# Performance work log

Hardware: AMD Instinct MI355X
Metric: run time of the kernel (lower is better)

## Reference

```python
import jax, jax.numpy as jnp
import numpy as np

BETA = 0.25  # commitment weight from __init__ default
K, D = 512, 64


def setup_inputs() -> dict:
    key = jax.random.key(0)
    k1, k2 = jax.random.split(key)
    latents = jax.random.normal(k1, (32, 64, 64, 64), dtype=jnp.float32)  # [B, D, H, W]
    # nn.Embedding weight initialized uniform(-1/K, 1/K)
    emb_weight = jax.random.uniform(k2, (K, D), dtype=jnp.float32, minval=-1.0 / K, maxval=1.0 / K)
    return {"latents": latents, "emb_weight": emb_weight, "validation": 1}


def reference(latents, emb_weight, validation):
    B, Dc, H, W = latents.shape
    lat = jnp.transpose(latents, (0, 2, 3, 1))          # [B, H, W, D]
    flat = lat.reshape(-1, Dc)                           # [N, D]
    # pairwise squared distances via sum-of-squares + matmul (as in source)
    dist = (jnp.sum(flat * flat, axis=1, keepdims=True)
            + jnp.sum(emb_weight * emb_weight, axis=1)
            - 2.0 * flat @ emb_weight.T)                 # [N, K]
    inds = jnp.argmin(dist, axis=1)                      # [N]
    # one_hot @ emb_weight == gather
    q = emb_weight[inds].reshape(B, H, W, Dc)            # [B, H, W, D]
    commitment_loss = jnp.mean((jax.lax.stop_gradient(q) - lat) ** 2)
    embedding_loss = jnp.mean((q - jax.lax.stop_gradient(lat)) ** 2)
    # eloss starts at 0.0 (and stays 0 in validation), so topology terms vanish
    vq_loss = commitment_loss * BETA + embedding_loss
    # straight-through estimator
    q_st = lat + jax.lax.stop_gradient(q - lat)
    return jnp.transpose(q_st, (0, 3, 1, 2)), vq_loss
```

## Files before the change

kernel.cpp:

```cpp
#include <hip/hip_runtime.h>


typedef __bf16 bf16_t;
typedef __attribute__((ext_vector_type(8))) __bf16 bf16x8;
typedef __attribute__((ext_vector_type(16))) float floatx16;

namespace {
constexpr int K    = 512;
constexpr int D    = 64;
constexpr int HW   = 4096;
constexpr int NPIX = 32 * HW;
constexpr int QOUT = NPIX * D;
constexpr int DEXT = 80;
}

__global__ void vq_prep(const float* __restrict__ emb,
                        bf16_t* __restrict__ ext,
                        float* __restrict__ loss) {
    int k = blockIdx.x * blockDim.x + threadIdx.x;
    if (k == 0) *loss = 0.0f;
    if (k < K) {
        float s = 0.0f;
        bf16_t row[DEXT];
#pragma unroll
        for (int d = 0; d < D; ++d) {
            float v = emb[k * D + d];
            s += v * v;
            row[d] = (bf16_t)v;
        }
        row[64] = (bf16_t)(-0.5f * s);
#pragma unroll
        for (int d = 65; d < DEXT; ++d) row[d] = (bf16_t)0.0f;
#pragma unroll
        for (int d = 0; d < DEXT; ++d) ext[k * DEXT + d] = row[d];
    }
}

__global__ __launch_bounds__(256) void vq_mfma(
    const float* __restrict__ lat,
    const float* __restrict__ emb,
    const bf16_t* __restrict__ ext,
    float* __restrict__ out,
    float* __restrict__ loss) {
    const int lane = threadIdx.x & 63;
    const int wave = threadIdx.x >> 6;
    const int col  = lane & 31;
    const int half = lane >> 5;
    const int n    = blockIdx.x * 128 + wave * 32 + col;
    const int b    = n >> 12;
    const int hw   = n & (HW - 1);
    const float* latp = lat + (size_t)b * D * HW + hw;

    float  xf[32];
    bf16x8 bfrag[5];
#pragma unroll
    for (int s = 0; s < 4; ++s) {
#pragma unroll
        for (int j = 0; j < 8; ++j) {
            int d = s * 16 + half * 8 + j;
            float v = latp[(size_t)d * HW];
            xf[s * 8 + j] = v;
            bfrag[s][j] = (bf16_t)v;
        }
    }
#pragma unroll
    for (int j = 0; j < 8; ++j) bfrag[4][j] = (bf16_t)0.0f;
    if (half == 0) bfrag[4][0] = (bf16_t)1.0f;

    float best  = -3.4e38f;
    int   bestk = 0;
    for (int t = 0; t < 16; ++t) {
        floatx16 acc;
#pragma unroll
        for (int r = 0; r < 16; ++r) acc[r] = 0.0f;
        const bf16_t* arow = ext + ((size_t)(t * 32 + col)) * DEXT + half * 8;
#pragma unroll
        for (int s = 0; s < 5; ++s) {
            bf16x8 afrag = *(const bf16x8*)(arow + s * 16);
            acc = __builtin_amdgcn_mfma_f32_32x32x16_bf16(afrag, bfrag[s], acc,
                                                          0, 0, 0);
        }
#pragma unroll
        for (int r = 0; r < 16; ++r) {
            if (acc[r] > best) {
                best  = acc[r];
                bestk = t * 32 + (r & 3) + 8 * (r >> 2) + 4 * half;
            }
        }
    }

    {
        float ob  = __shfl_xor(best, 32, 64);
        int   obk = __shfl_xor(bestk, 32, 64);
        if (ob > best || (ob == best && obk < bestk)) { best = ob; bestk = obk; }
    }

    const float* eb   = emb + bestk * D + half * 8;
    float* outp       = out + (size_t)b * D * HW + hw;
    float  sq = 0.0f;
#pragma unroll
    for (int s = 0; s < 4; ++s) {
        float4 q0 = *(const float4*)(eb + s * 16);
        float4 q1 = *(const float4*)(eb + s * 16 + 4);
        float d0 = q0.x - xf[s * 8 + 0], d1 = q0.y - xf[s * 8 + 1];
        float d2 = q0.z - xf[s * 8 + 2], d3 = q0.w - xf[s * 8 + 3];
        float d4 = q1.x - xf[s * 8 + 4], d5 = q1.y - xf[s * 8 + 5];
        float d6 = q1.z - xf[s * 8 + 6], d7 = q1.w - xf[s * 8 + 7];
        sq += d0 * d0 + d1 * d1 + d2 * d2 + d3 * d3;
        sq += d4 * d4 + d5 * d5 + d6 * d6 + d7 * d7;
        const int dbase = s * 16 + half * 8;
        outp[(size_t)(dbase + 0) * HW] = q0.x;
        outp[(size_t)(dbase + 1) * HW] = q0.y;
        outp[(size_t)(dbase + 2) * HW] = q0.z;
        outp[(size_t)(dbase + 3) * HW] = q0.w;
        outp[(size_t)(dbase + 4) * HW] = q1.x;
        outp[(size_t)(dbase + 5) * HW] = q1.y;
        outp[(size_t)(dbase + 6) * HW] = q1.z;
        outp[(size_t)(dbase + 7) * HW] = q1.w;
    }

#pragma unroll
    for (int off = 32; off > 0; off >>= 1) sq += __shfl_down(sq, off, 64);
    __shared__ float part[4];
    if (lane == 0) part[wave] = sq;
    __syncthreads();
    if (threadIdx.x == 0) {
        float t = part[0] + part[1] + part[2] + part[3];
        atomicAdd(loss, t * (1.25f / (float)QOUT));
    }
}

extern "C" void kernel_launch(void* const* d_in, const int* in_sizes, int n_in,
                              void* d_out, int out_size, void* d_ws, size_t ws_size,
                              hipStream_t stream) {
    const float* lat = (const float*)d_in[0];
    const float* emb = (const float*)d_in[1];
    float* out       = (float*)d_out;
    float* loss      = out + QOUT;
    bf16_t* ext      = (bf16_t*)d_ws;

    vq_prep<<<2, 256, 0, stream>>>(emb, ext, loss);
    vq_mfma<<<NPIX / 128, 256, 0, stream>>>(lat, emb, ext, out, loss);
}
```

Baseline: 116.5 us.

## Process two pixel groups per wave to reuse codebook fragments across MFMAs

Each wave now handles 64 pixels as two 32-pixel groups. Every codebook A-fragment it loads feeds two MFMA chains, which halves codebook fetches per pixel and exposes more independent MFMA work. To save registers, the fp32 latent copy is dropped and the loss term is computed from the bf16-rounded latents, which slightly changes loss precision. The prep kernel is also vectorised with float4 loads and bf16x8 stores, and the grid is halved to match.

```diff
diff --git a/kernel.cpp b/kernel.cpp
--- a/kernel.cpp
+++ b/kernel.cpp
@@ -12,28 +12,37 @@
 constexpr int NPIX = 32 * HW;
 constexpr int QOUT = NPIX * D;
 constexpr int DEXT = 80;
+constexpr int G    = 2;
 }
 
-__global__ void vq_prep(const float* __restrict__ emb,
-                        bf16_t* __restrict__ ext,
-                        float* __restrict__ loss) {
-    int k = blockIdx.x * blockDim.x + threadIdx.x;
+__global__ __launch_bounds__(64) void vq_prep(const float* __restrict__ emb,
+                                              bf16_t* __restrict__ ext,
+                                              float* __restrict__ loss) {
+    int k = blockIdx.x * 64 + threadIdx.x;
     if (k == 0) *loss = 0.0f;
-    if (k < K) {
-        float s = 0.0f;
-        bf16_t row[DEXT];
+    if (k >= K) return;
+    const float4* row = (const float4*)(emb + k * D);
+    float4 v[16];
 #pragma unroll
-        for (int d = 0; d < D; ++d) {
-            float v = emb[k * D + d];
-            s += v * v;
-            row[d] = (bf16_t)v;
-        }
-        row[64] = (bf16_t)(-0.5f * s);
+    for (int i = 0; i < 16; ++i) v[i] = row[i];
+    float s = 0.0f;
 #pragma unroll
-        for (int d = 65; d < DEXT; ++d) row[d] = (bf16_t)0.0f;
+    for (int i = 0; i < 16; ++i)
+        s += v[i].x * v[i].x + v[i].y * v[i].y + v[i].z * v[i].z + v[i].w * v[i].w;
+    bf16_t r[DEXT];
 #pragma unroll
-        for (int d = 0; d < DEXT; ++d) ext[k * DEXT + d] = row[d];
+    for (int i = 0; i < 16; ++i) {
+        r[4 * i + 0] = (bf16_t)v[i].x;
+        r[4 * i + 1] = (bf16_t)v[i].y;
+        r[4 * i + 2] = (bf16_t)v[i].z;
+        r[4 * i + 3] = (bf16_t)v[i].w;
     }
+    r[64] = (bf16_t)(-0.5f * s);
+#pragma unroll
+    for (int i = 65; i < DEXT; ++i) r[i] = (bf16_t)0.0f;
+#pragma unroll
+    for (int i = 0; i < DEXT / 8; ++i)
+        ((bf16x8*)(ext + k * DEXT))[i] = *(const bf16x8*)(r + 8 * i);
 }
 
 __global__ __launch_bounds__(256) void vq_mfma(
@@ -46,83 +55,104 @@
     const int wave = threadIdx.x >> 6;
     const int col  = lane & 31;
     const int half = lane >> 5;
-    const int n    = blockIdx.x * 128 + wave * 32 + col;
-    const int b    = n >> 12;
-    const int hw   = n & (HW - 1);
-    const float* latp = lat + (size_t)b * D * HW + hw;
+    const int nb   = blockIdx.x * (64 * G * 4) / 2 + wave * 64;
 
-    float  xf[32];
-    bf16x8 bfrag[5];
+    int bg[G], hwg[G];
+    bf16x8 bfrag[G][5];
 #pragma unroll
-    for (int s = 0; s < 4; ++s) {
+    for (int g = 0; g < G; ++g) {
+        int n = nb + g * 32 + col;
+        bg[g] = n >> 12;
+        hwg[g] = n & (HW - 1);
+        const float* latp = lat + (size_t)bg[g] * D * HW + hwg[g];
 #pragma unroll
-        for (int j = 0; j < 8; ++j) {
-            int d = s * 16 + half * 8 + j;
-            float v = latp[(size_t)d * HW];
-            xf[s * 8 + j] = v;
-            bfrag[s][j] = (bf16_t)v;
-        }
-    }
+        for (int s = 0; s < 4; ++s) {
 #pragma unroll
-    for (int j = 0; j < 8; ++j) bfrag[4][j] = (bf16_t)0.0f;
-    if (half == 0) bfrag[4][0] = (bf16_t)1.0f;
-
-    float best  = -3.4e38f;
-    int   bestk = 0;
-    for (int t = 0; t < 16; ++t) {
-        floatx16 acc;
-#pragma unroll
-        for (int r = 0; r < 16; ++r) acc[r] = 0.0f;
-        const bf16_t* arow = ext + ((size_t)(t * 32 + col)) * DEXT + half * 8;
-#pragma unroll
-        for (int s = 0; s < 5; ++s) {
-            bf16x8 afrag = *(const bf16x8*)(arow + s * 16);
-            acc = __builtin_amdgcn_mfma_f32_32x32x16_bf16(afrag, bfrag[s], acc,
-                                                          0, 0, 0);
+            for (int j = 0; j < 8; ++j) {
+                int d = s * 16 + half * 8 + j;
+                bfrag[g][s][j] = (bf16_t)latp[(size_t)d * HW];
+            }
         }
 #pragma unroll
-        for (int r = 0; r < 16; ++r) {
-            if (acc[r] > best) {
-                best  = acc[r];
-                bestk = t * 32 + (r & 3) + 8 * (r >> 2) + 4 * half;
+        for (int j = 0; j < 8; ++j) bfrag[g][4][j] = (bf16_t)0.0f;
+        if (half == 0) bfrag[g][4][0] = (bf16_t)1.0f;
+    }
+
+    float best[G];
+    int   bestk[G];
+#pragma unroll
+    for (int g = 0; g < G; ++g) { best[g] = -3.4e38f; bestk[g] = 0; }
+
+#pragma unroll 4
+    for (int t = 0; t < 16; ++t) {
+        const bf16_t* arow = ext + ((size_t)(t * 32 + col)) * DEXT + half * 8;
+        bf16x8 af[5];
+#pragma unroll
+        for (int s = 0; s < 5; ++s) af[s] = *(const bf16x8*)(arow + s * 16);
+
+        floatx16 acc[G];
+#pragma unroll
+        for (int g = 0; g < G; ++g) {
+#pragma unroll
+            for (int r = 0; r < 16; ++r) acc[g][r] = 0.0f;
+#pragma unroll
+            for (int s = 0; s < 5; ++s)
+                acc[g] = __builtin_amdgcn_mfma_f32_32x32x16_bf16(
+                    af[s], bfrag[g][s], acc[g], 0, 0, 0);
+        }
+#pragma unroll
+        for (int g = 0; g < G; ++g) {
+#pragma unroll
+            for (int r = 0; r < 16; ++r) {
+                if (acc[g][r] > best[g]) {
+                    best[g]  = acc[g][r];
+                    bestk[g] = t * 32 + (r & 3) + 8 * (r >> 2) + 4 * half;
+                }
             }
         }
     }
 
-    {
-        float ob  = __shfl_xor(best, 32, 64);
-        int   obk = __shfl_xor(bestk, 32, 64);
-        if (ob > best || (ob == best && obk < bestk)) { best = ob; bestk = obk; }
-    }
+    float sqtot = 0.0f;
+#pragma unroll
+    for (int g = 0; g < G; ++g) {
+        float ob  = __shfl_xor(best[g], 32, 64);
+        int   obk = __shfl_xor(bestk[g], 32, 64);
+        if (ob > best[g] || (ob == best[g] && obk < bestk[g])) {
+            best[g] = ob; bestk[g] = obk;
+        }
 
-    const float* eb   = emb + bestk * D + half * 8;
-    float* outp       = out + (size_t)b * D * HW + hw;
-    float  sq = 0.0f;
+        const float* eb = emb + bestk[g] * D + half * 8;
+        float* outp     = out + (size_t)bg[g] * D * HW + hwg[g];
+        float sq = 0.0f;
 #pragma unroll
-    for (int s = 0; s < 4; ++s) {
-        float4 q0 = *(const float4*)(eb + s * 16);
-        float4 q1 = *(const float4*)(eb + s * 16 + 4);
-        float d0 = q0.x - xf[s * 8 + 0], d1 = q0.y - xf[s * 8 + 1];
-        float d2 = q0.z - xf[s * 8 + 2], d3 = q0.w - xf[s * 8 + 3];
-        float d4 = q1.x - xf[s * 8 + 4], d5 = q1.y - xf[s * 8 + 5];
-        float d6 = q1.z - xf[s * 8 + 6], d7 = q1.w - xf[s * 8 + 7];
-        sq += d0 * d0 + d1 * d1 + d2 * d2 + d3 * d3;
-        sq += d4 * d4 + d5 * d5 + d6 * d6 + d7 * d7;
-        const int dbase = s * 16 + half * 8;
-        outp[(size_t)(dbase + 0) * HW] = q0.x;
-        outp[(size_t)(dbase + 1) * HW] = q0.y;
-        outp[(size_t)(dbase + 2) * HW] = q0.z;
-        outp[(size_t)(dbase + 3) * HW] = q0.w;
-        outp[(size_t)(dbase + 4) * HW] = q1.x;
-        outp[(size_t)(dbase + 5) * HW] = q1.y;
-        outp[(size_t)(dbase + 6) * HW] = q1.z;
-        outp[(size_t)(dbase + 7) * HW] = q1.w;
+        for (int s = 0; s < 4; ++s) {
+            float4 q0 = *(const float4*)(eb + s * 16);
+            float4 q1 = *(const float4*)(eb + s * 16 + 4);
+            float x0 = (float)bfrag[g][s][0], x1 = (float)bfrag[g][s][1];
+            float x2 = (float)bfrag[g][s][2], x3 = (float)bfrag[g][s][3];
+            float x4 = (float)bfrag[g][s][4], x5 = (float)bfrag[g][s][5];
+            float x6 = (float)bfrag[g][s][6], x7 = (float)bfrag[g][s][7];
+            float d0 = q0.x - x0, d1 = q0.y - x1, d2 = q0.z - x2, d3 = q0.w - x3;
+            float d4 = q1.x - x4, d5 = q1.y - x5, d6 = q1.z - x6, d7 = q1.w - x7;
+            sq += d0 * d0 + d1 * d1 + d2 * d2 + d3 * d3;
+            sq += d4 * d4 + d5 * d5 + d6 * d6 + d7 * d7;
+            const int dbase = s * 16 + half * 8;
+            outp[(size_t)(dbase + 0) * HW] = q0.x;
+            outp[(size_t)(dbase + 1) * HW] = q0.y;
+            outp[(size_t)(dbase + 2) * HW] = q0.z;
+            outp[(size_t)(dbase + 3) * HW] = q0.w;
+            outp[(size_t)(dbase + 4) * HW] = q1.x;
+            outp[(size_t)(dbase + 5) * HW] = q1.y;
+            outp[(size_t)(dbase + 6) * HW] = q1.z;
+            outp[(size_t)(dbase + 7) * HW] = q1.w;
+        }
+        sqtot += sq;
     }
 
 #pragma unroll
-    for (int off = 32; off > 0; off >>= 1) sq += __shfl_down(sq, off, 64);
+    for (int off = 32; off > 0; off >>= 1) sqtot += __shfl_down(sqtot, off, 64);
     __shared__ float part[4];
-    if (lane == 0) part[wave] = sq;
+    if (lane == 0) part[wave] = sqtot;
     __syncthreads();
     if (threadIdx.x == 0) {
         float t = part[0] + part[1] + part[2] + part[3];
@@ -139,6 +169,6 @@
     float* loss      = out + QOUT;
     bf16_t* ext      = (bf16_t*)d_ws;
 
-    vq_prep<<<2, 256, 0, stream>>>(emb, ext, loss);
-    vq_mfma<<<NPIX / 128, 256, 0, stream>>>(lat, emb, ext, out, loss);
+    vq_prep<<<K / 64, 64, 0, stream>>>(emb, ext, loss);
+    vq_mfma<<<NPIX / 256, 256, 0, stream>>>(lat, emb, ext, out, loss);
 }
```

New measurement: 108.1 us. 1.08x faster.
